# Kernel optimization log

Measured on AMD Instinct MI355X. Metric: run time of the kernel, lower is better.

## Reference

```python
import jax, jax.numpy as jnp
import numpy as np

N = 100000          # number of nodes (nums)
E = 1200000         # nnz of the normalized adjacency
D = 64              # embed_size; layer_size = [64, 64, 64]
NODE_DROP = 0.1     # args.node_dropout[0]
MESS_DROP = (0.1, 0.1, 0.1)
EPS = 1e-12         # F.normalize eps


def setup_inputs() -> dict:
    key = jax.random.key(0)
    ks = jax.random.split(key, 10)
    rows = jax.random.randint(ks[0], (E,), 0, N, dtype=jnp.int32)
    cols = jax.random.randint(ks[1], (E,), 0, N, dtype=jnp.int32)
    vals = jax.random.uniform(ks[2], (E,), dtype=jnp.float32)
    emb = jax.random.normal(ks[3], (N, D), dtype=jnp.float32) * 0.1
    W0 = jax.random.normal(ks[4], (D, D), dtype=jnp.float32) * 0.1
    b0 = jax.random.normal(ks[5], (1, D), dtype=jnp.float32) * 0.1
    W1 = jax.random.normal(ks[6], (D, D), dtype=jnp.float32) * 0.1
    b1 = jax.random.normal(ks[7], (1, D), dtype=jnp.float32) * 0.1
    W2 = jax.random.normal(ks[8], (D, D), dtype=jnp.float32) * 0.1
    b2 = jax.random.normal(ks[9], (1, D), dtype=jnp.float32) * 0.1
    return dict(rows=rows, cols=cols, vals=vals, emb=emb,
                W0=W0, b0=b0, W1=W1, b1=b1, W2=W2, b2=b2)


def reference(rows, cols, vals, emb, W0, b0, W1, b1, W2, b2):
    drop_key = jax.random.key(42)
    k_node, k0, k1, k2 = jax.random.split(drop_key, 4)

    # sparse node dropout: zero dropped edge values (== removing nnz), scale survivors
    keep_e = jax.random.bernoulli(k_node, 1.0 - NODE_DROP, (E,))
    a_vals = jnp.where(keep_e, vals / (1.0 - NODE_DROP), 0.0)

    def layer(ego, W, b, rate, k):
        # SpMM: out[r] += a_vals * ego[c]   (COO scatter-add)
        side = jax.ops.segment_sum(a_vals[:, None] * ego[cols], rows, num_segments=N)
        h = side @ W + b
        keep = jax.random.bernoulli(k, 1.0 - rate, h.shape)
        h = jnp.where(keep, h / (1.0 - rate), 0.0)          # mess dropout
        nrm = h / jnp.maximum(jnp.linalg.norm(h, axis=1, keepdims=True), EPS)
        return h, nrm  # ego continues as the (un-normalized) dropped output

    all_embs = [emb]
    ego = emb
    for (W, b, rate, k) in ((W0, b0, MESS_DROP[0], k0),
                            (W1, b1, MESS_DROP[1], k1),
                            (W2, b2, MESS_DROP[2], k2)):
        ego, nrm = layer(ego, W, b, rate, k)
        all_embs.append(nrm)
    return jnp.concatenate(all_embs, axis=1)  # [N, 4*D]
```

## Files before the change

kernel.cpp:

```cpp
#include <hip/hip_runtime.h>
#include <stdint.h>

#define N_NODES 100000
#define DIM 64
#define E_EDGES 1200000
#define NBK 6250
#define NREP 8
#define BCAP_R 64
#define ROW_CAP 40
#define BPB 16

__host__ __device__ __forceinline__ void tf2x32(uint32_t k0, uint32_t k1,
                                                uint32_t c0, uint32_t c1,
                                                uint32_t& o0, uint32_t& o1) {
    uint32_t ks2 = k0 ^ k1 ^ 0x1BD11BDAu;
    uint32_t x0 = c0 + k0, x1 = c1 + k1;
#define TF_RND(r) { x0 += x1; x1 = (x1 << r) | (x1 >> (32 - r)); x1 ^= x0; }
    TF_RND(13) TF_RND(15) TF_RND(26) TF_RND(6)
    x0 += k1;  x1 += ks2 + 1u;
    TF_RND(17) TF_RND(29) TF_RND(16) TF_RND(24)
    x0 += ks2; x1 += k0 + 2u;
    TF_RND(13) TF_RND(15) TF_RND(26) TF_RND(6)
    x0 += k0;  x1 += k1 + 3u;
    TF_RND(17) TF_RND(29) TF_RND(16) TF_RND(24)
    x0 += k1;  x1 += ks2 + 4u;
    TF_RND(13) TF_RND(15) TF_RND(26) TF_RND(6)
    x0 += ks2; x1 += k0 + 5u;
#undef TF_RND
    o0 = x0; o1 = x1;
}

__device__ __forceinline__ bool keep_bit(uint32_t k0, uint32_t k1, uint32_t idx) {
    uint32_t y0, y1;
    tf2x32(k0, k1, 0u, idx, y0, y1);
    return (((y0 ^ y1) >> 9) < 7549747u);
}

__device__ __forceinline__ uint16_t f2bf(float f) {
    uint32_t x = __float_as_uint(f);
    return (uint16_t)((x + 0x7fffu + ((x >> 16) & 1u)) >> 16);
}

__global__ void k_embcvt(const float* __restrict__ emb, float* __restrict__ out,
                         uint16_t* __restrict__ egoA, int* __restrict__ bcnt) {
    int gid = blockIdx.x * blockDim.x + threadIdx.x;
    if (gid < NREP * NBK) bcnt[gid] = 0;
    int stride = gridDim.x * blockDim.x;
    const int total = N_NODES * 16;
    for (int i = gid; i < total; i += stride) {
        int n = i >> 4, q = i & 15;
        float4 v = ((const float4*)emb)[(size_t)n * 16 + q];
        ((float4*)out)[(size_t)n * 64 + q] = v;
        ushort4 bb;
        bb.x = f2bf(v.x); bb.y = f2bf(v.y); bb.z = f2bf(v.z); bb.w = f2bf(v.w);
        ((ushort4*)egoA)[(size_t)n * 16 + q] = bb;
    }
}

__global__ void k_bucket(const int* __restrict__ rows, const int* __restrict__ cols,
                         const float* __restrict__ vals, int* __restrict__ bcnt,
                         int2* __restrict__ bedge, uint32_t k0, uint32_t k1) {
    int rep = blockIdx.x & (NREP - 1);
    int i = blockIdx.x * blockDim.x + threadIdx.x;
    int stride = gridDim.x * blockDim.x;
    for (; i < E_EDGES; i += stride) {
        if (keep_bit(k0, k1, (uint32_t)i)) {
            int r = rows[i];
            int b = r >> 4;
            int rl = r & 15;
            int cell = rep * NBK + b;
            int pos = atomicAdd(&bcnt[cell], 1);
            if (pos < BCAP_R)
                bedge[(size_t)cell * BCAP_R + pos] =
                    make_int2((rl << 17) | cols[i],
                              __float_as_int(vals[i] * (1.0f / 0.9f)));
        }
    }
}

__global__ __launch_bounds__(256) void k_bin(const int2* __restrict__ bedge,
                                             const int* __restrict__ bcnt,
                                             uint32_t* __restrict__ pairs,
                                             int* __restrict__ cnt) {
    __shared__ uint32_t lp[256 * ROW_CAP];
    __shared__ int lc[256];
    __shared__ int lcc[BPB * NREP];
    int blk = blockIdx.x, t = threadIdx.x;
    for (int i = t; i < 256 * ROW_CAP / 4; i += 256)
        ((uint4*)lp)[i] = make_uint4(0u, 0u, 0u, 0u);
    lc[t] = 0;
    int b0 = blk * BPB;
    if (t < BPB * NREP) {
        int lb = t >> 3, rep = t & 7;
        int ne = bcnt[rep * NBK + b0 + lb];
        lcc[t] = (ne > BCAP_R) ? BCAP_R : ne;
    }
    __syncthreads();
    int e = t & 63, wv = t >> 6;
    for (int cc = 0; cc < BPB * NREP; cc += 4) {
        int cell = cc + wv;
        int lb = cell >> 3, rep = cell & 7;
        int ne = lcc[cell];
        if (e < ne) {
            int2 en = bedge[((size_t)(rep * NBK + b0 + lb)) * BCAP_R + e];
            uint32_t meta = (uint32_t)en.x;
            int rl = (int)(meta >> 17);
            uint32_t col = meta & 0x1FFFFu;
            float v = __int_as_float(en.y);
            int rloc = lb * 16 + rl;
            int pos = atomicAdd(&lc[rloc], 1);
            if (pos < ROW_CAP) {
                uint32_t q = (uint32_t)(v * 16384.0f + 0.5f);
                lp[rloc * ROW_CAP + pos] = (q << 17) | col;
            }
        }
    }
    __syncthreads();
    int nrows = N_NODES - blk * 256;
    if (nrows > 256) nrows = 256;
    int nq = nrows * ROW_CAP / 4;
    uint4* dst = (uint4*)(pairs + (size_t)blk * 256 * ROW_CAP);
    const uint4* src = (const uint4*)lp;
    for (int i = t; i < nq; i += 256) dst[i] = src[i];
    if (t < nrows) cnt[blk * 256 + t] = lc[t];
}

#define GATHER_FMA(V, aE, aO)                                              \
    {                                                                      \
        uint32_t c0 = V.x & 0x1FFFFu;  float a0 = (float)(V.x >> 17) * S;  \
        uint32_t c1 = V.y & 0x1FFFFu;  float a1 = (float)(V.y >> 17) * S;  \
        uint32_t c2 = V.z & 0x1FFFFu;  float a2 = (float)(V.z >> 17) * S;  \
        uint32_t c3 = V.w & 0x1FFFFu;  float a3 = (float)(V.w >> 17) * S;  \
        uint32_t u0 = egoU[c0 * 32u + (uint32_t)l2];                       \
        uint32_t u1 = egoU[c1 * 32u + (uint32_t)l2];                       \
        uint32_t u2 = egoU[c2 * 32u + (uint32_t)l2];                       \
        uint32_t u3 = egoU[c3 * 32u + (uint32_t)l2];                       \
        aE = fmaf(a0, __uint_as_float(u0 << 16), aE);                      \
        aO = fmaf(a0, __uint_as_float(u0 & 0xffff0000u), aO);              \
        aE = fmaf(a1, __uint_as_float(u1 << 16), aE);                      \
        aO = fmaf(a1, __uint_as_float(u1 & 0xffff0000u), aO);              \
        aE = fmaf(a2, __uint_as_float(u2 << 16), aE);                      \
        aO = fmaf(a2, __uint_as_float(u2 & 0xffff0000u), aO);              \
        aE = fmaf(a3, __uint_as_float(u3 << 16), aE);                      \
        aO = fmaf(a3, __uint_as_float(u3 & 0xffff0000u), aO);              \
    }

__global__ __launch_bounds__(256, 6) void k_spmm(
    const int* __restrict__ cnt, const uint32_t* __restrict__ pairs,
    const uint16_t* __restrict__ ego_in, float* __restrict__ side) {
    int t = threadIdx.x;
    int w = t >> 6, lane = t & 63;
    int l2 = lane & 31;
    int hi4 = (lane >> 5) << 2;
    const float S = 1.0f / 16384.0f;
    const uint32_t* egoU = (const uint32_t*)ego_in;
    int wid0 = blockIdx.x * 4 + w;
    const int NW = 2048 * 4;
    const int NQ = N_NODES / 4;
    for (int q = wid0; q < NQ; q += NW) {
        int un = __builtin_amdgcn_readfirstlane(q * 4);
        int l0 = cnt[un + 0], l1 = cnt[un + 1], l2c = cnt[un + 2], l3 = cnt[un + 3];
        const uint32_t* rp = pairs + (size_t)un * ROW_CAP + hi4;
        uint4 A0 = *reinterpret_cast<const uint4*>(rp);
        uint4 A1 = *reinterpret_cast<const uint4*>(rp + ROW_CAP);
        uint4 A2 = *reinterpret_cast<const uint4*>(rp + 2 * ROW_CAP);
        uint4 A3 = *reinterpret_cast<const uint4*>(rp + 3 * ROW_CAP);
        uint4 B0 = *reinterpret_cast<const uint4*>(rp + 8);
        uint4 B1 = *reinterpret_cast<const uint4*>(rp + ROW_CAP + 8);
        uint4 B2 = *reinterpret_cast<const uint4*>(rp + 2 * ROW_CAP + 8);
        uint4 B3 = *reinterpret_cast<const uint4*>(rp + 3 * ROW_CAP + 8);
        float aE0 = 0.f, aO0 = 0.f, aE1 = 0.f, aO1 = 0.f;
        float aE2 = 0.f, aO2 = 0.f, aE3 = 0.f, aO3 = 0.f;
        GATHER_FMA(A0, aE0, aO0)
        GATHER_FMA(A1, aE1, aO1)
        GATHER_FMA(A2, aE2, aO2)
        GATHER_FMA(A3, aE3, aO3)
        GATHER_FMA(B0, aE0, aO0)
        GATHER_FMA(B1, aE1, aO1)
        GATHER_FMA(B2, aE2, aO2)
        GATHER_FMA(B3, aE3, aO3)
        int n0 = (l0 + 7) & ~7;  if (n0 > ROW_CAP) n0 = ROW_CAP;
        int n1 = (l1 + 7) & ~7;  if (n1 > ROW_CAP) n1 = ROW_CAP;
        int n2 = (l2c + 7) & ~7; if (n2 > ROW_CAP) n2 = ROW_CAP;
        int n3 = (l3 + 7) & ~7;  if (n3 > ROW_CAP) n3 = ROW_CAP;
        int jmax = n0;
        if (n1 > jmax) jmax = n1;
        if (n2 > jmax) jmax = n2;
        if (n3 > jmax) jmax = n3;
        if (jmax > 16) {
            const uint4 zed = make_uint4(0u, 0u, 0u, 0u);
            for (int j = 16; j < jmax; j += 8) {
                uint4 V0 = (j < n0) ? *reinterpret_cast<const uint4*>(rp + j) : zed;
                uint4 V1 = (j < n1) ? *reinterpret_cast<const uint4*>(rp + ROW_CAP + j) : zed;
                uint4 V2 = (j < n2) ? *reinterpret_cast<const uint4*>(rp + 2 * ROW_CAP + j) : zed;
                uint4 V3 = (j < n3) ? *reinterpret_cast<const uint4*>(rp + 3 * ROW_CAP + j) : zed;
                GATHER_FMA(V0, aE0, aO0)
                GATHER_FMA(V1, aE1, aO1)
                GATHER_FMA(V2, aE2, aO2)
                GATHER_FMA(V3, aE3, aO3)
            }
        }
        aE0 += __shfl_xor(aE0, 32, 64);  aO0 += __shfl_xor(aO0, 32, 64);
        aE1 += __shfl_xor(aE1, 32, 64);  aO1 += __shfl_xor(aO1, 32, 64);
        aE2 += __shfl_xor(aE2, 32, 64);  aO2 += __shfl_xor(aO2, 32, 64);
        aE3 += __shfl_xor(aE3, 32, 64);  aO3 += __shfl_xor(aO3, 32, 64);
        int nsel = (lane >> 5) * 2;
        float2 vA = (lane < 32) ? make_float2(aE0, aO0) : make_float2(aE2, aO2);
        float2 vB = (lane < 32) ? make_float2(aE1, aO1) : make_float2(aE3, aO3);
        reinterpret_cast<float2*>(side + (size_t)(un + nsel) * DIM)[l2] = vA;
        reinterpret_cast<float2*>(side + (size_t)(un + nsel + 1) * DIM)[l2] = vB;
    }
}

__global__ __launch_bounds__(256, 4) void k_epi(
    const float* __restrict__ side,
    const float* __restrict__ W, const float* __restrict__ bias,
    uint16_t* __restrict__ h_out,
    float* __restrict__ out, int coloff,
    uint32_t k0, uint32_t k1) {
    __shared__ float sS[4][64];
    int t = threadIdx.x;
    int w = t >> 6, lane = t & 63;
    float wreg[64];
#pragma unroll
    for (int k = 0; k < 64; ++k)
        wreg[k] = W[k * 64 + lane];
    float breg = bias[lane];
    int wid0 = blockIdx.x * 4 + w;
    const int NW = 2048 * 4;
    for (int n = wid0; n < N_NODES; n += NW) {
        int un = __builtin_amdgcn_readfirstlane(n);
        float acc = side[(size_t)un * DIM + lane];
        sS[w][lane] = acc;
        float h = breg;
        const float4* s4p = reinterpret_cast<const float4*>(&sS[w][0]);
#pragma unroll
        for (int kq = 0; kq < 16; ++kq) {
            float4 s4 = s4p[kq];
            h = fmaf(s4.x, wreg[4 * kq + 0], h);
            h = fmaf(s4.y, wreg[4 * kq + 1], h);
            h = fmaf(s4.z, wreg[4 * kq + 2], h);
            h = fmaf(s4.w, wreg[4 * kq + 3], h);
        }
        h = keep_bit(k0, k1, (uint32_t)un * 64u + (uint32_t)lane) ? h * (1.0f / 0.9f) : 0.0f;
        float s = h * h;
#pragma unroll
        for (int o = 32; o > 0; o >>= 1) s += __shfl_xor(s, o, 64);
        float nv = h / fmaxf(sqrtf(s), 1e-12f);
        if (h_out) h_out[(size_t)un * DIM + lane] = f2bf(h);
        out[(size_t)un * 256 + coloff + lane] = nv;
    }
}

extern "C" void kernel_launch(void* const* d_in, const int* in_sizes, int n_in,
                              void* d_out, int out_size, void* d_ws, size_t ws_size,
                              hipStream_t stream) {
    const int*   rows = (const int*)d_in[0];
    const int*   cols = (const int*)d_in[1];
    const float* vals = (const float*)d_in[2];
    const float* emb  = (const float*)d_in[3];
    const float* Wk[3] = { (const float*)d_in[4], (const float*)d_in[6], (const float*)d_in[8] };
    const float* bk[3] = { (const float*)d_in[5], (const float*)d_in[7], (const float*)d_in[9] };
    float* out = (float*)d_out;

    int*      bcnt  = (int*)d_ws;
    int*      cnt   = bcnt + 65536;
    int2*     bedge = (int2*)(cnt + 100000 + 14);
    bedge = (int2*)(((uintptr_t)bedge + 511) & ~(uintptr_t)511);
    uint32_t* pairs = (uint32_t*)(bedge + (size_t)NREP * NBK * BCAP_R);
    float*    side  = (float*)(pairs + (size_t)N_NODES * ROW_CAP);
    uint16_t* egoA  = (uint16_t*)(side + (size_t)N_NODES * DIM);
    uint16_t* egoB  = egoA + (size_t)N_NODES * DIM;

    uint32_t kn[2], kl[3][2];
    tf2x32(0u, 42u, 0u, 0u, kn[0], kn[1]);
    tf2x32(0u, 42u, 0u, 1u, kl[0][0], kl[0][1]);
    tf2x32(0u, 42u, 0u, 2u, kl[1][0], kl[1][1]);
    tf2x32(0u, 42u, 0u, 3u, kl[2][0], kl[2][1]);

    k_embcvt<<<2048, 256, 0, stream>>>(emb, out, egoA, bcnt);
    k_bucket<<<2048, 256, 0, stream>>>(rows, cols, vals, bcnt, bedge, kn[0], kn[1]);
    k_bin<<<(NBK + BPB - 1) / BPB, 256, 0, stream>>>(bedge, bcnt, pairs, cnt);

    k_spmm<<<2048, 256, 0, stream>>>(cnt, pairs, egoA, side);
    k_epi<<<2048, 256, 0, stream>>>(side, Wk[0], bk[0], egoB, out, 64,
                                    kl[0][0], kl[0][1]);
    k_spmm<<<2048, 256, 0, stream>>>(cnt, pairs, egoB, side);
    k_epi<<<2048, 256, 0, stream>>>(side, Wk[1], bk[1], egoA, out, 128,
                                    kl[1][0], kl[1][1]);
    k_spmm<<<2048, 256, 0, stream>>>(cnt, pairs, egoA, side);
    k_epi<<<2048, 256, 0, stream>>>(side, Wk[2], bk[2], nullptr, out, 192,
                                    kl[2][0], kl[2][1]);
}
```

Measured before the change: 256.2 us.

## Partition row edges by column range and sweep SpMM one column quarter at a time

The binning kernel now counts each row's edges per column quarter (col>>15), pads each segment to even length, and stores the segment boundaries packed in one word per row. The SpMM kernel gives each wave up to four quads of rows and processes all of them for one column range before moving to the next. The aim is to keep the ego rows being gathered within a smaller window that fits better in cache. Each lane now gathers one bf16 element per edge instead of a packed pair, and ROW_CAP grows to 48. This adds a second pass over the bucketed edges and more per-edge load instructions, and truncation now happens per segment.

```diff
diff --git a/kernel.cpp b/kernel.cpp
--- a/kernel.cpp
+++ b/kernel.cpp
@@ -7,8 +7,10 @@
 #define NBK 6250
 #define NREP 8
 #define BCAP_R 64
-#define ROW_CAP 40
+#define ROW_CAP 48
 #define BPB 16
+#define NQUAD 25000
+#define NWAVE 8192
 
 __host__ __device__ __forceinline__ void tf2x32(uint32_t k0, uint32_t k1,
                                                 uint32_t c0, uint32_t c1,
@@ -40,6 +42,9 @@
     uint32_t x = __float_as_uint(f);
     return (uint16_t)((x + 0x7fffu + ((x >> 16) & 1u)) >> 16);
 }
+__device__ __forceinline__ float bf2f(uint16_t u) {
+    return __uint_as_float(((uint32_t)u) << 16);
+}
 
 __global__ void k_embcvt(const float* __restrict__ emb, float* __restrict__ out,
                          uint16_t* __restrict__ egoA, int* __restrict__ bcnt) {
@@ -81,14 +86,15 @@
 __global__ __launch_bounds__(256) void k_bin(const int2* __restrict__ bedge,
                                              const int* __restrict__ bcnt,
                                              uint32_t* __restrict__ pairs,
-                                             int* __restrict__ cnt) {
+                                             uint32_t* __restrict__ cnt4) {
     __shared__ uint32_t lp[256 * ROW_CAP];
-    __shared__ int lc[256];
+    __shared__ int lc4[256 * 4];
+    __shared__ int lcur[256 * 4];
     __shared__ int lcc[BPB * NREP];
     int blk = blockIdx.x, t = threadIdx.x;
     for (int i = t; i < 256 * ROW_CAP / 4; i += 256)
         ((uint4*)lp)[i] = make_uint4(0u, 0u, 0u, 0u);
-    lc[t] = 0;
+    for (int i = t; i < 1024; i += 256) lc4[i] = 0;
     int b0 = blk * BPB;
     if (t < BPB * NREP) {
         int lb = t >> 3, rep = t & 7;
@@ -106,9 +112,41 @@
             uint32_t meta = (uint32_t)en.x;
             int rl = (int)(meta >> 17);
             uint32_t col = meta & 0x1FFFFu;
+            atomicAdd(&lc4[(lb * 16 + rl) * 4 + (int)(col >> 15)], 1);
+        }
+    }
+    __syncthreads();
+    {
+        int c0 = lc4[t * 4 + 0], c1 = lc4[t * 4 + 1];
+        int c2 = lc4[t * 4 + 2], c3 = lc4[t * 4 + 3];
+        int p0 = (c0 + 1) & ~1, p1 = (c1 + 1) & ~1;
+        int p2 = (c2 + 1) & ~1, p3 = (c3 + 1) & ~1;
+        int s1 = p0; if (s1 > ROW_CAP) s1 = ROW_CAP;
+        int s2 = s1 + p1; if (s2 > ROW_CAP) s2 = ROW_CAP;
+        int s3 = s2 + p2; if (s3 > ROW_CAP) s3 = ROW_CAP;
+        int tot = s3 + p3; if (tot > ROW_CAP) tot = ROW_CAP;
+        lcur[t * 4 + 0] = 0;
+        lcur[t * 4 + 1] = s1;
+        lcur[t * 4 + 2] = s2;
+        lcur[t * 4 + 3] = s3;
+        int grow = blk * 256 + t;
+        if (grow < N_NODES)
+            cnt4[grow] = (uint32_t)s1 | ((uint32_t)s2 << 8) |
+                         ((uint32_t)s3 << 16) | ((uint32_t)tot << 24);
+    }
+    __syncthreads();
+    for (int cc = 0; cc < BPB * NREP; cc += 4) {
+        int cell = cc + wv;
+        int lb = cell >> 3, rep = cell & 7;
+        int ne = lcc[cell];
+        if (e < ne) {
+            int2 en = bedge[((size_t)(rep * NBK + b0 + lb)) * BCAP_R + e];
+            uint32_t meta = (uint32_t)en.x;
+            int rl = (int)(meta >> 17);
+            uint32_t col = meta & 0x1FFFFu;
             float v = __int_as_float(en.y);
             int rloc = lb * 16 + rl;
-            int pos = atomicAdd(&lc[rloc], 1);
+            int pos = atomicAdd(&lcur[rloc * 4 + (int)(col >> 15)], 1);
             if (pos < ROW_CAP) {
                 uint32_t q = (uint32_t)(v * 16384.0f + 0.5f);
                 lp[rloc * ROW_CAP + pos] = (q << 17) | col;
@@ -122,93 +160,84 @@
     uint4* dst = (uint4*)(pairs + (size_t)blk * 256 * ROW_CAP);
     const uint4* src = (const uint4*)lp;
     for (int i = t; i < nq; i += 256) dst[i] = src[i];
-    if (t < nrows) cnt[blk * 256 + t] = lc[t];
-}
-
-#define GATHER_FMA(V, aE, aO)                                              \
-    {                                                                      \
-        uint32_t c0 = V.x & 0x1FFFFu;  float a0 = (float)(V.x >> 17) * S;  \
-        uint32_t c1 = V.y & 0x1FFFFu;  float a1 = (float)(V.y >> 17) * S;  \
-        uint32_t c2 = V.z & 0x1FFFFu;  float a2 = (float)(V.z >> 17) * S;  \
-        uint32_t c3 = V.w & 0x1FFFFu;  float a3 = (float)(V.w >> 17) * S;  \
-        uint32_t u0 = egoU[c0 * 32u + (uint32_t)l2];                       \
-        uint32_t u1 = egoU[c1 * 32u + (uint32_t)l2];                       \
-        uint32_t u2 = egoU[c2 * 32u + (uint32_t)l2];                       \
-        uint32_t u3 = egoU[c3 * 32u + (uint32_t)l2];                       \
-        aE = fmaf(a0, __uint_as_float(u0 << 16), aE);                      \
-        aO = fmaf(a0, __uint_as_float(u0 & 0xffff0000u), aO);              \
-        aE = fmaf(a1, __uint_as_float(u1 << 16), aE);                      \
-        aO = fmaf(a1, __uint_as_float(u1 & 0xffff0000u), aO);              \
-        aE = fmaf(a2, __uint_as_float(u2 << 16), aE);                      \
-        aO = fmaf(a2, __uint_as_float(u2 & 0xffff0000u), aO);              \
-        aE = fmaf(a3, __uint_as_float(u3 << 16), aE);                      \
-        aO = fmaf(a3, __uint_as_float(u3 & 0xffff0000u), aO);              \
-    }
+}
 
 __global__ __launch_bounds__(256, 6) void k_spmm(
-    const int* __restrict__ cnt, const uint32_t* __restrict__ pairs,
+    const uint32_t* __restrict__ cnt4, const uint32_t* __restrict__ pairs,
     const uint16_t* __restrict__ ego_in, float* __restrict__ side) {
     int t = threadIdx.x;
     int w = t >> 6, lane = t & 63;
-    int l2 = lane & 31;
-    int hi4 = (lane >> 5) << 2;
     const float S = 1.0f / 16384.0f;
-    const uint32_t* egoU = (const uint32_t*)ego_in;
-    int wid0 = blockIdx.x * 4 + w;
-    const int NW = 2048 * 4;
-    const int NQ = N_NODES / 4;
-    for (int q = wid0; q < NQ; q += NW) {
-        int un = __builtin_amdgcn_readfirstlane(q * 4);
-        int l0 = cnt[un + 0], l1 = cnt[un + 1], l2c = cnt[un + 2], l3 = cnt[un + 3];
-        const uint32_t* rp = pairs + (size_t)un * ROW_CAP + hi4;
-        uint4 A0 = *reinterpret_cast<const uint4*>(rp);
-        uint4 A1 = *reinterpret_cast<const uint4*>(rp + ROW_CAP);
-        uint4 A2 = *reinterpret_cast<const uint4*>(rp + 2 * ROW_CAP);
-        uint4 A3 = *reinterpret_cast<const uint4*>(rp + 3 * ROW_CAP);
-        uint4 B0 = *reinterpret_cast<const uint4*>(rp + 8);
-        uint4 B1 = *reinterpret_cast<const uint4*>(rp + ROW_CAP + 8);
-        uint4 B2 = *reinterpret_cast<const uint4*>(rp + 2 * ROW_CAP + 8);
-        uint4 B3 = *reinterpret_cast<const uint4*>(rp + 3 * ROW_CAP + 8);
-        float aE0 = 0.f, aO0 = 0.f, aE1 = 0.f, aO1 = 0.f;
-        float aE2 = 0.f, aO2 = 0.f, aE3 = 0.f, aO3 = 0.f;
-        GATHER_FMA(A0, aE0, aO0)
-        GATHER_FMA(A1, aE1, aO1)
-        GATHER_FMA(A2, aE2, aO2)
-        GATHER_FMA(A3, aE3, aO3)
-        GATHER_FMA(B0, aE0, aO0)
-        GATHER_FMA(B1, aE1, aO1)
-        GATHER_FMA(B2, aE2, aO2)
-        GATHER_FMA(B3, aE3, aO3)
-        int n0 = (l0 + 7) & ~7;  if (n0 > ROW_CAP) n0 = ROW_CAP;
-        int n1 = (l1 + 7) & ~7;  if (n1 > ROW_CAP) n1 = ROW_CAP;
-        int n2 = (l2c + 7) & ~7; if (n2 > ROW_CAP) n2 = ROW_CAP;
-        int n3 = (l3 + 7) & ~7;  if (n3 > ROW_CAP) n3 = ROW_CAP;
-        int jmax = n0;
-        if (n1 > jmax) jmax = n1;
-        if (n2 > jmax) jmax = n2;
-        if (n3 > jmax) jmax = n3;
-        if (jmax > 16) {
-            const uint4 zed = make_uint4(0u, 0u, 0u, 0u);
-            for (int j = 16; j < jmax; j += 8) {
-                uint4 V0 = (j < n0) ? *reinterpret_cast<const uint4*>(rp + j) : zed;
-                uint4 V1 = (j < n1) ? *reinterpret_cast<const uint4*>(rp + ROW_CAP + j) : zed;
-                uint4 V2 = (j < n2) ? *reinterpret_cast<const uint4*>(rp + 2 * ROW_CAP + j) : zed;
-                uint4 V3 = (j < n3) ? *reinterpret_cast<const uint4*>(rp + 3 * ROW_CAP + j) : zed;
-                GATHER_FMA(V0, aE0, aO0)
-                GATHER_FMA(V1, aE1, aO1)
-                GATHER_FMA(V2, aE2, aO2)
-                GATHER_FMA(V3, aE3, aO3)
+    int wid = blockIdx.x * 4 + w;
+    float acc[4][4];
+#pragma unroll
+    for (int k = 0; k < 4; ++k)
+#pragma unroll
+        for (int i = 0; i < 4; ++i) acc[k][i] = 0.f;
+    uint32_t cv[4][4];
+#pragma unroll
+    for (int k = 0; k < 4; ++k) {
+        int q = wid + k * NWAVE;
+        if (q < NQUAD) {
+            int un = __builtin_amdgcn_readfirstlane(q * 4);
+#pragma unroll
+            for (int i = 0; i < 4; ++i) cv[k][i] = cnt4[un + i];
+        } else {
+#pragma unroll
+            for (int i = 0; i < 4; ++i) cv[k][i] = 0u;
+        }
+    }
+    for (int r = 0; r < 4; ++r) {
+#pragma unroll
+        for (int k = 0; k < 4; ++k) {
+            int q = wid + k * NWAVE;
+            if (q >= NQUAD) continue;
+            int un = __builtin_amdgcn_readfirstlane(q * 4);
+            const uint32_t* base = pairs + (size_t)un * ROW_CAP;
+            int st[4], en[4];
+#pragma unroll
+            for (int i = 0; i < 4; ++i) {
+                uint32_t c = cv[k][i];
+                st[i] = (r == 0) ? 0 : (int)((c >> (8 * (r - 1))) & 0xFFu);
+                en[i] = (int)((c >> (8 * r)) & 0xFFu);
             }
-        }
-        aE0 += __shfl_xor(aE0, 32, 64);  aO0 += __shfl_xor(aO0, 32, 64);
-        aE1 += __shfl_xor(aE1, 32, 64);  aO1 += __shfl_xor(aO1, 32, 64);
-        aE2 += __shfl_xor(aE2, 32, 64);  aO2 += __shfl_xor(aO2, 32, 64);
-        aE3 += __shfl_xor(aE3, 32, 64);  aO3 += __shfl_xor(aO3, 32, 64);
-        int nsel = (lane >> 5) * 2;
-        float2 vA = (lane < 32) ? make_float2(aE0, aO0) : make_float2(aE2, aO2);
-        float2 vB = (lane < 32) ? make_float2(aE1, aO1) : make_float2(aE3, aO3);
-        reinterpret_cast<float2*>(side + (size_t)(un + nsel) * DIM)[l2] = vA;
-        reinterpret_cast<float2*>(side + (size_t)(un + nsel + 1) * DIM)[l2] = vB;
+            int jmax = en[0] - st[0];
+            if (en[1] - st[1] > jmax) jmax = en[1] - st[1];
+            if (en[2] - st[2] > jmax) jmax = en[2] - st[2];
+            if (en[3] - st[3] > jmax) jmax = en[3] - st[3];
+            for (int j = 0; j < jmax; j += 2) {
+#pragma unroll
+                for (int i = 0; i < 4; ++i) {
+                    int off = st[i] + j;
+                    bool valid = off < en[i];
+                    int offc = valid ? off : 0;
+                    uint2 P = *reinterpret_cast<const uint2*>(base + i * ROW_CAP + offc);
+                    if (!valid) { P.x = 0u; P.y = 0u; }
+                    {
+                        uint32_t col = P.x & 0x1FFFFu;
+                        float a = (float)(P.x >> 17) * S;
+                        uint16_t u = ego_in[(size_t)col * DIM + lane];
+                        acc[k][i] = fmaf(a, bf2f(u), acc[k][i]);
+                    }
+                    {
+                        uint32_t col = P.y & 0x1FFFFu;
+                        float a = (float)(P.y >> 17) * S;
+                        uint16_t u = ego_in[(size_t)col * DIM + lane];
+                        acc[k][i] = fmaf(a, bf2f(u), acc[k][i]);
+                    }
+                }
+            }
+        }
+    }
+#pragma unroll
+    for (int k = 0; k < 4; ++k) {
+        int q = wid + k * NWAVE;
+        if (q < NQUAD) {
+            int un = q * 4;
+#pragma unroll
+            for (int i = 0; i < 4; ++i)
+                side[(size_t)(un + i) * DIM + lane] = acc[k][i];
+        }
     }
 }
 
@@ -264,8 +293,8 @@
     float* out = (float*)d_out;
 
     int*      bcnt  = (int*)d_ws;
-    int*      cnt   = bcnt + 65536;
-    int2*     bedge = (int2*)(cnt + 100000 + 14);
+    uint32_t* cnt4  = (uint32_t*)(bcnt + 65536);
+    int2*     bedge = (int2*)(cnt4 + 100000 + 14);
     bedge = (int2*)(((uintptr_t)bedge + 511) & ~(uintptr_t)511);
     uint32_t* pairs = (uint32_t*)(bedge + (size_t)NREP * NBK * BCAP_R);
     float*    side  = (float*)(pairs + (size_t)N_NODES * ROW_CAP);
@@ -280,15 +309,15 @@
 
     k_embcvt<<<2048, 256, 0, stream>>>(emb, out, egoA, bcnt);
     k_bucket<<<2048, 256, 0, stream>>>(rows, cols, vals, bcnt, bedge, kn[0], kn[1]);
-    k_bin<<<(NBK + BPB - 1) / BPB, 256, 0, stream>>>(bedge, bcnt, pairs, cnt);
-
-    k_spmm<<<2048, 256, 0, stream>>>(cnt, pairs, egoA, side);
+    k_bin<<<(NBK + BPB - 1) / BPB, 256, 0, stream>>>(bedge, bcnt, pairs, cnt4);
+
+    k_spmm<<<2048, 256, 0, stream>>>(cnt4, pairs, egoA, side);
     k_epi<<<2048, 256, 0, stream>>>(side, Wk[0], bk[0], egoB, out, 64,
                                     kl[0][0], kl[0][1]);
-    k_spmm<<<2048, 256, 0, stream>>>(cnt, pairs, egoB, side);
+    k_spmm<<<2048, 256, 0, stream>>>(cnt4, pairs, egoB, side);
     k_epi<<<2048, 256, 0, stream>>>(side, Wk[1], bk[1], egoA, out, 128,
                                     kl[1][0], kl[1][1]);
-    k_spmm<<<2048, 256, 0, stream>>>(cnt, pairs, egoA, side);
+    k_spmm<<<2048, 256, 0, stream>>>(cnt4, pairs, egoA, side);
     k_epi<<<2048, 256, 0, stream>>>(side, Wk[2], bk[2], nullptr, out, 192,
                                     kl[2][0], kl[2][1]);
 }
```

Measured after the change: 432.8 us. 1.69x slower.
